# Performance work log

Hardware: AMD Instinct MI355X
Metric: run time of the kernel (lower is better)

## Reference

```python
import jax, jax.numpy as jnp
import numpy as np

B, S = 4, 2048
D_MODEL, N_HEADS, D_KV = 1024, 16, 64
NUM_BUCKETS, MAX_DIST = 32, 128


def _relative_position_bucket(relative_position, num_buckets=NUM_BUCKETS, max_distance=MAX_DIST):
    # bidirectional (encoder) variant, faithful to FlaxT5Attention._relative_position_bucket
    num_buckets = num_buckets // 2
    relative_buckets = (relative_position > 0).astype(jnp.int32) * num_buckets
    rp = jnp.abs(relative_position)
    max_exact = num_buckets // 2
    is_small = rp < max_exact
    rp_large = max_exact + (
        jnp.log(rp.astype(jnp.float32) / max_exact)
        / np.log(max_distance / max_exact)
        * (num_buckets - max_exact)
    )
    rp_large = jnp.minimum(rp_large, num_buckets - 1)
    return relative_buckets + jnp.where(is_small, rp, rp_large.astype(jnp.int32))


def setup_inputs() -> dict:
    key = jax.random.key(0)
    ks = jax.random.split(key, 6)
    return {
        "hidden_states": jax.random.normal(ks[0], (B, S, D_MODEL), jnp.float32),
        "mask": jnp.zeros((B, S), jnp.float32),  # additive mask, 0 = attend
        "wq": jax.random.normal(ks[1], (D_MODEL, N_HEADS * D_KV), jnp.float32) * 0.02,
        "wk": jax.random.normal(ks[2], (D_MODEL, N_HEADS * D_KV), jnp.float32) * 0.02,
        "wv": jax.random.normal(ks[3], (D_MODEL, N_HEADS * D_KV), jnp.float32) * 0.02,
        "wo": jax.random.normal(ks[4], (N_HEADS * D_KV, D_MODEL), jnp.float32) * 0.02,
        "rel_bias": jax.random.normal(ks[5], (NUM_BUCKETS, N_HEADS), jnp.float32) * 0.02,
    }


def reference(hidden_states, mask, wq, wk, wv, wo, rel_bias):
    b, s, _ = hidden_states.shape
    # QKV projections, split heads -> [B, S, H, D]
    q = (hidden_states @ wq).reshape(b, s, N_HEADS, D_KV)
    k = (hidden_states @ wk).reshape(b, s, N_HEADS, D_KV)
    v = (hidden_states @ wv).reshape(b, s, N_HEADS, D_KV)

    # relative position bias -> [1, H, S, S]
    pos = jnp.arange(s, dtype=jnp.int32)
    relative_position = pos[None, :] - pos[:, None]  # memory - query
    buckets = _relative_position_bucket(relative_position)
    position_bias = rel_bias[buckets].transpose(2, 0, 1)[None]  # [1,H,S,S]
    # encoder path: additive mask expanded to [B,1,1,K]
    position_bias = position_bias + mask[:, None, None, :]

    # flax dot_product_attention_weights scales q by 1/sqrt(depth)
    scores = jnp.einsum("bqhd,bkhd->bhqk", q / jnp.sqrt(jnp.float32(D_KV)), k)
    attn_weights = jax.nn.softmax(scores + position_bias, axis=-1)

    attn_output = jnp.einsum("bhqk,bkhd->bqhd", attn_weights, v)
    attn_output = attn_output.reshape(b, s, N_HEADS * D_KV) @ wo
    return attn_output, position_bias
```

## Files before the change

### kernel.cpp

```cpp
#include <hip/hip_runtime.h>
#include <hip/hip_bf16.h>

typedef __attribute__((ext_vector_type(8))) short bf16x8;
typedef __attribute__((ext_vector_type(8))) unsigned short u16x8;
typedef __attribute__((ext_vector_type(4))) float f32x4;

#define B_   4
#define S_   2048
#define H_   16
#define DKV  64
#define DM   1024

static __device__ __forceinline__ f32x4 mfma16(bf16x8 a, bf16x8 b, f32x4 c){
  return __builtin_amdgcn_mfma_f32_16x16x32_bf16(a, b, c, 0, 0, 0);
}
static __device__ __forceinline__ unsigned short f2b(float f){
  union { __hip_bfloat16 b; unsigned short u; } x;
  x.b = __float2bfloat16(f);
  return x.u;
}

__global__ void cast_h_kernel(const float* __restrict__ in, unsigned short* __restrict__ out, int n4){
  int i = blockIdx.x * 256 + threadIdx.x;
  if (i >= n4) return;
  float4 v = reinterpret_cast<const float4*>(in)[i];
  ushort4 r;
  r.x = f2b(v.x); r.y = f2b(v.y); r.z = f2b(v.z); r.w = f2b(v.w);
  reinterpret_cast<ushort4*>(out)[i] = r;
}

__global__ void transpose_w_kernel(const float* __restrict__ w0, const float* __restrict__ w1,
                                   const float* __restrict__ w2, const float* __restrict__ w3,
                                   unsigned short* o0, unsigned short* o1,
                                   unsigned short* o2, unsigned short* o3){
  int z = blockIdx.z;
  const float* src = (z==0) ? w0 : (z==1) ? w1 : (z==2) ? w2 : w3;
  unsigned short* dst = (z==0) ? o0 : (z==1) ? o1 : (z==2) ? o2 : o3;
  __shared__ float tile[32][33];
  int bx = blockIdx.x * 32, by = blockIdx.y * 32;
  int tx = threadIdx.x, ty = threadIdx.y;
  #pragma unroll
  for (int i = 0; i < 32; i += 8)
    tile[ty + i][tx] = src[(size_t)(by + ty + i) * DM + bx + tx];
  __syncthreads();
  #pragma unroll
  for (int i = 0; i < 32; i += 8)
    dst[(size_t)(bx + ty + i) * DM + by + tx] = f2b(tile[tx][ty + i]);
}

__global__ void build_table_kernel(const float* __restrict__ rel_bias, float* __restrict__ table_t){
  int i = blockIdx.x * 256 + threadIdx.x;
  if (i >= 16 * 4095) return;
  int h = i / 4095;
  int idx = i - h * 4095;
  int rel = idx - 2047;
  int bucket = (rel > 0) ? 16 : 0;
  int rp = (rel < 0) ? -rel : rel;
  int off;
  if (rp < 8) off = rp;
  else off = 8 + (rp>=12) + (rp>=16) + (rp>=23) + (rp>=32) + (rp>=46) + (rp>=64) + (rp>=91);
  table_t[i] = rel_bias[(bucket + off) * 16 + h];
}

__global__ void posbias_kernel(const float* __restrict__ relb, const float* __restrict__ mask,
                               float* __restrict__ out){
  __shared__ float rbh[32];
  int row = blockIdx.x;
  int q = row & (S_ - 1);
  int h = (row >> 11) & (H_ - 1);
  int b = row >> 15;
  int tid = threadIdx.x;
  if (tid < 32) rbh[tid] = relb[tid * 16 + h];
  __syncthreads();
  const float* mrow = mask + b * S_;
  float* orow = out + (size_t)row * S_;
  int k0 = tid * 8;
  #pragma unroll
  for (int c = 0; c < 2; ++c){
    float4 mv = *(const float4*)(mrow + k0 + c * 4);
    float4 v;
    #pragma unroll
    for (int j = 0; j < 4; ++j){
      int k = k0 + c * 4 + j;
      int rel = k - q;
      int bucket = (rel > 0) ? 16 : 0;
      int rp = (rel < 0) ? -rel : rel;
      int off = (rp < 8) ? rp
              : 8 + (rp>=12) + (rp>=16) + (rp>=23) + (rp>=32) + (rp>=46) + (rp>=64) + (rp>=91);
      (&v.x)[j] = rbh[bucket + off] + (&mv.x)[j];
    }
    *(float4*)(orow + k0 + c*4) = v;
  }
}

template<int MODE>
__global__ __launch_bounds__(256, 2) void gemm_bt_kernel(
    const unsigned short* __restrict__ A, const unsigned short* __restrict__ Bt,
    void* __restrict__ outp, int M, int N, int K, float scale)
{
  __shared__ __align__(16) unsigned short As[128 * 40];
  __shared__ __align__(16) unsigned short Bs[128 * 40];
  int tid = threadIdx.x; int lane = tid & 63; int w = tid >> 6;
  int wr = w >> 1, wc = w & 1;
  int n0 = blockIdx.x * 128, m0 = blockIdx.y * 128;
  const char* Ab = (const char*)A;
  const char* Bb = (const char*)Bt;
  size_t Kb = (size_t)K * 2;

  int srow = (tid * 16) >> 6;
  int scolb = (tid * 16) & 63;

  f32x4 acc[4][4];
  #pragma unroll
  for (int i = 0; i < 4; ++i)
    #pragma unroll
    for (int j = 0; j < 4; ++j) acc[i][j] = (f32x4){0.f, 0.f, 0.f, 0.f};

  bf16x8 ar[2], br[2];
  auto gload = [&](int kt){
    size_t k0b = (size_t)kt * 64;
    #pragma unroll
    for (int c = 0; c < 2; ++c){
      int row = srow + c * 64;
      ar[c] = *(const bf16x8*)(Ab + (size_t)(m0 + row) * Kb + k0b + scolb);
      br[c] = *(const bf16x8*)(Bb + (size_t)(n0 + row) * Kb + k0b + scolb);
    }
  };
  auto lwrite = [&](){
    #pragma unroll
    for (int c = 0; c < 2; ++c){
      int row = srow + c * 64;
      *(bf16x8*)((char*)As + row * 80 + scolb) = ar[c];
      *(bf16x8*)((char*)Bs + row * 80 + scolb) = br[c];
    }
  };

  int nk = K >> 5;
  gload(0);
  lwrite();
  for (int kt = 0; kt < nk; ++kt){
    __syncthreads();
    if (kt + 1 < nk) gload(kt + 1);
    bf16x8 af[4], bfr[4];
    #pragma unroll
    for (int f = 0; f < 4; ++f){
      int row = wr * 64 + f * 16 + (lane & 15);
      af[f] = *(const bf16x8*)((const char*)As + row * 80 + (lane >> 4) * 16);
    }
    #pragma unroll
    for (int f = 0; f < 4; ++f){
      int row = wc * 64 + f * 16 + (lane & 15);
      bfr[f] = *(const bf16x8*)((const char*)Bs + row * 80 + (lane >> 4) * 16);
    }
    #pragma unroll
    for (int i = 0; i < 4; ++i)
      #pragma unroll
      for (int j = 0; j < 4; ++j)
        acc[i][j] = mfma16(af[i], bfr[j], acc[i][j]);
    __syncthreads();
    if (kt + 1 < nk) lwrite();
  }

  #pragma unroll
  for (int i = 0; i < 4; ++i){
    #pragma unroll
    for (int j = 0; j < 4; ++j){
      #pragma unroll
      for (int r = 0; r < 4; ++r){
        int m = m0 + wr * 64 + i * 16 + ((lane >> 4) * 4) + r;
        int n = n0 + wc * 64 + j * 16 + (lane & 15);
        float v = acc[i][j][r] * scale;
        if (MODE == 0){
          ((float*)outp)[(size_t)m * N + n] = v;
        } else {
          int b = m >> 11, s = m & 2047, hh = n >> 6, d = n & 63;
          ((unsigned short*)outp)[(((size_t)(b * H_ + hh) * S_) + s) * DKV + d] = f2b(v);
        }
      }
    }
  }
}

__global__ __launch_bounds__(256, 2) void attn_mfma_kernel(
    const unsigned short* __restrict__ Qp, const unsigned short* __restrict__ Kp,
    const unsigned short* __restrict__ Vp, const float* __restrict__ table_t,
    const float* __restrict__ mask, unsigned short* __restrict__ outp)
{
  __shared__ __align__(16) unsigned short Ks[64][72];
  __shared__ __align__(16) unsigned short Vs[64][72];
  __shared__ __align__(16) unsigned short Ps[4][16][72];
  __shared__ float bias_s[127];
  __shared__ float mask_s[64];

  int bid = blockIdx.x;
  int qt = bid & 31; int h = (bid >> 5) & 15; int b = bid >> 9;
  int qb = qt * 64;
  const unsigned short* qptr = Qp + ((size_t)(b * H_ + h) * S_ + qb) * DKV;
  const unsigned short* kptr = Kp + (size_t)(b * H_ + h) * S_ * DKV;
  const unsigned short* vptr = Vp + (size_t)(b * H_ + h) * S_ * DKV;
  int tid = threadIdx.x; int lane = tid & 63; int w = tid >> 6;

  bf16x8 qf[2];
  {
    const unsigned short* qrow = qptr + (size_t)(w * 16 + (lane & 15)) * DKV + 8 * (lane >> 4);
    qf[0] = *(const bf16x8*)qrow;
    qf[1] = *(const bf16x8*)(qrow + 32);
  }
  float m_r[4], l_r[4];
  f32x4 o_acc[4];
  #pragma unroll
  for (int r = 0; r < 4; ++r){ m_r[r] = -1e30f; l_r[r] = 0.f; }
  #pragma unroll
  for (int d = 0; d < 4; ++d) o_acc[d] = (f32x4){0.f, 0.f, 0.f, 0.f};

  int bias_base = h * 4095 + (2047 - qb - 63);

  int skey = tid & 63;
  int sd0  = (tid >> 6) * 16;

  for (int k0 = 0; k0 < S_; k0 += 64){
    const unsigned short* krow = kptr + (size_t)(k0 + skey) * DKV + sd0;
    const unsigned short* vrow = vptr + (size_t)(k0 + skey) * DKV + sd0;
    u16x8 ka = *(const u16x8*)krow;
    u16x8 kb2 = *(const u16x8*)(krow + 8);
    u16x8 va = *(const u16x8*)vrow;
    u16x8 vb2 = *(const u16x8*)(vrow + 8);
    float biasr = (tid < 127) ? table_t[bias_base + k0 + tid] : 0.f;
    float maskr = (tid >= 128 && tid < 192) ? mask[b * S_ + k0 + (tid - 128)] : 0.f;

    __syncthreads();
    *(u16x8*)&Ks[skey][sd0]     = ka;
    *(u16x8*)&Ks[skey][sd0 + 8] = kb2;
    #pragma unroll
    for (int j = 0; j < 8; ++j){
      Vs[sd0 + j][skey]     = va[j];
      Vs[sd0 + 8 + j][skey] = vb2[j];
    }
    if (tid < 127) bias_s[tid] = biasr;
    else if (tid < 192) mask_s[tid - 128] = maskr;
    __syncthreads();

    f32x4 sc[4];
    #pragma unroll
    for (int kb = 0; kb < 4; ++kb){
      sc[kb] = (f32x4){0.f, 0.f, 0.f, 0.f};
      #pragma unroll
      for (int ks = 0; ks < 2; ++ks){
        int row = kb * 16 + (lane & 15);
        bf16x8 kf = *(const bf16x8*)&Ks[row][ks * 32 + (lane >> 4) * 8];
        sc[kb] = mfma16(qf[ks], kf, sc[kb]);
      }
    }
    float t[4][4];
    float tmax[4] = {-1e30f, -1e30f, -1e30f, -1e30f};
    #pragma unroll
    for (int kb = 0; kb < 4; ++kb){
      int k_l = kb * 16 + (lane & 15);
      float mk = mask_s[k_l];
      #pragma unroll
      for (int r = 0; r < 4; ++r){
        int q_l = w * 16 + (lane >> 4) * 4 + r;
        float tv = sc[kb][r] + bias_s[k_l - q_l + 63] + mk;
        t[kb][r] = tv;
        tmax[r] = fmaxf(tmax[r], tv);
      }
    }
    #pragma unroll
    for (int r = 0; r < 4; ++r){
      #pragma unroll
      for (int off = 1; off < 16; off <<= 1)
        tmax[r] = fmaxf(tmax[r], __shfl_xor(tmax[r], off, 64));
    }
    float scl[4];
    #pragma unroll
    for (int r = 0; r < 4; ++r){
      float mn = fmaxf(m_r[r], tmax[r]);
      scl[r] = __expf(m_r[r] - mn);
      m_r[r] = mn;
    }
    float rs[4] = {0.f, 0.f, 0.f, 0.f};
    #pragma unroll
    for (int kb = 0; kb < 4; ++kb)
      #pragma unroll
      for (int r = 0; r < 4; ++r){
        float p = __expf(t[kb][r] - m_r[r]);
        t[kb][r] = p;
        rs[r] += p;
      }
    #pragma unroll
    for (int r = 0; r < 4; ++r){
      #pragma unroll
      for (int off = 1; off < 16; off <<= 1)
        rs[r] += __shfl_xor(rs[r], off, 64);
      l_r[r] = l_r[r] * scl[r] + rs[r];
      o_acc[0][r] *= scl[r]; o_acc[1][r] *= scl[r];
      o_acc[2][r] *= scl[r]; o_acc[3][r] *= scl[r];
    }
    #pragma unroll
    for (int kb = 0; kb < 4; ++kb)
      #pragma unroll
      for (int r = 0; r < 4; ++r){
        int prow = (lane >> 4) * 4 + r;
        int pcol = kb * 16 + (lane & 15);
        Ps[w][prow][pcol] = f2b(t[kb][r]);
      }
    bf16x8 pa[2];
    #pragma unroll
    for (int ks = 0; ks < 2; ++ks)
      pa[ks] = *(const bf16x8*)&Ps[w][lane & 15][ks * 32 + (lane >> 4) * 8];
    #pragma unroll
    for (int db = 0; db < 4; ++db)
      #pragma unroll
      for (int ks = 0; ks < 2; ++ks){
        bf16x8 vf = *(const bf16x8*)&Vs[db * 16 + (lane & 15)][ks * 32 + (lane >> 4) * 8];
        o_acc[db] = mfma16(pa[ks], vf, o_acc[db]);
      }
  }

  #pragma unroll
  for (int r = 0; r < 4; ++r){
    float inv = 1.0f / l_r[r];
    int qg = qb + w * 16 + (lane >> 4) * 4 + r;
    size_t rowoff = ((size_t)b * S_ + qg) * DM + h * DKV;
    #pragma unroll
    for (int db = 0; db < 4; ++db)
      outp[rowoff + db * 16 + (lane & 15)] = f2b(o_acc[db][r] * inv);
  }
}

extern "C" void kernel_launch(void* const* d_in, const int* in_sizes, int n_in,
                              void* d_out, int out_size, void* d_ws, size_t ws_size,
                              hipStream_t stream) {
  const float* hs   = (const float*)d_in[0];
  const float* msk  = (const float*)d_in[1];
  const float* wq   = (const float*)d_in[2];
  const float* wk   = (const float*)d_in[3];
  const float* wv   = (const float*)d_in[4];
  const float* wo   = (const float*)d_in[5];
  const float* relb = (const float*)d_in[6];

  float* out_attn = (float*)d_out;
  float* out_pb   = (float*)d_out + (size_t)B_ * S_ * DM;
  char* ws = (char*)out_pb;

  unsigned short* h_bf = (unsigned short*)(ws + 0);
  unsigned short* wq_t = (unsigned short*)(ws + 16777216);
  unsigned short* wk_t = (unsigned short*)(ws + 18874368);
  unsigned short* wv_t = (unsigned short*)(ws + 20971520);
  unsigned short* wo_t = (unsigned short*)(ws + 23068672);
  unsigned short* q_b  = (unsigned short*)(ws + 25165824);
  unsigned short* k_b  = (unsigned short*)(ws + 41943040);
  unsigned short* v_b  = (unsigned short*)(ws + 58720256);
  float*          tabl = (float*)(ws + 75497472);

  cast_h_kernel<<<8192, 256, 0, stream>>>(hs, h_bf, (B_ * S_ * DM) / 4);
  transpose_w_kernel<<<dim3(32, 32, 4), dim3(32, 8), 0, stream>>>(wq, wk, wv, wo,
                                                                  wq_t, wk_t, wv_t, wo_t);
  build_table_kernel<<<256, 256, 0, stream>>>(relb, tabl);

  gemm_bt_kernel<1><<<dim3(8, 64), 256, 0, stream>>>(h_bf, wq_t, q_b, 8192, 1024, 1024, 0.125f);
  gemm_bt_kernel<1><<<dim3(8, 64), 256, 0, stream>>>(h_bf, wk_t, k_b, 8192, 1024, 1024, 1.0f);
  gemm_bt_kernel<1><<<dim3(8, 64), 256, 0, stream>>>(h_bf, wv_t, v_b, 8192, 1024, 1024, 1.0f);

  attn_mfma_kernel<<<B_ * H_ * 32, 256, 0, stream>>>(q_b, k_b, v_b, tabl, msk, h_bf);

  gemm_bt_kernel<0><<<dim3(8, 64), 256, 0, stream>>>(h_bf, wo_t, out_attn, 8192, 1024, 1024, 1.0f);

  posbias_kernel<<<B_ * H_ * S_, 256, 0, stream>>>(relb, msk, out_pb);
}
```

Baseline: 540.8 us.

## Fuse QKV projections into one GEMM and prefetch K/V tiles in attention

```diff
diff --git a/kernel.cpp b/kernel.cpp
--- a/kernel.cpp
+++ b/kernel.cpp
@@ -169,12 +169,14 @@
       for (int r = 0; r < 4; ++r){
         int m = m0 + wr * 64 + i * 16 + ((lane >> 4) * 4) + r;
         int n = n0 + wc * 64 + j * 16 + (lane & 15);
-        float v = acc[i][j][r] * scale;
         if (MODE == 0){
-          ((float*)outp)[(size_t)m * N + n] = v;
+          ((float*)outp)[(size_t)m * N + n] = acc[i][j][r] * scale;
         } else {
-          int b = m >> 11, s = m & 2047, hh = n >> 6, d = n & 63;
-          ((unsigned short*)outp)[(((size_t)(b * H_ + hh) * S_) + s) * DKV + d] = f2b(v);
+          int sel = n >> 10, nn = n & 1023;
+          float v = acc[i][j][r] * (sel == 0 ? 0.125f : 1.0f);
+          int b = m >> 11, s = m & 2047, hh = nn >> 6, d = nn & 63;
+          ((unsigned short*)outp)[(size_t)sel * 8388608 +
+              (((size_t)(b * H_ + hh) * S_) + s) * DKV + d] = f2b(v);
         }
       }
     }
@@ -218,17 +220,19 @@
   int skey = tid & 63;
   int sd0  = (tid >> 6) * 16;
 
-  for (int k0 = 0; k0 < S_; k0 += 64){
+  u16x8 ka, kb2, va, vb2;
+  float biasr = 0.f, maskr = 0.f;
+  auto gload = [&](int k0){
     const unsigned short* krow = kptr + (size_t)(k0 + skey) * DKV + sd0;
     const unsigned short* vrow = vptr + (size_t)(k0 + skey) * DKV + sd0;
-    u16x8 ka = *(const u16x8*)krow;
-    u16x8 kb2 = *(const u16x8*)(krow + 8);
-    u16x8 va = *(const u16x8*)vrow;
-    u16x8 vb2 = *(const u16x8*)(vrow + 8);
-    float biasr = (tid < 127) ? table_t[bias_base + k0 + tid] : 0.f;
-    float maskr = (tid >= 128 && tid < 192) ? mask[b * S_ + k0 + (tid - 128)] : 0.f;
-
-    __syncthreads();
+    ka  = *(const u16x8*)krow;
+    kb2 = *(const u16x8*)(krow + 8);
+    va  = *(const u16x8*)vrow;
+    vb2 = *(const u16x8*)(vrow + 8);
+    if (tid < 127) biasr = table_t[bias_base + k0 + tid];
+    else if (tid >= 128 && tid < 192) maskr = mask[b * S_ + k0 + (tid - 128)];
+  };
+  auto lwrite = [&](){
     *(u16x8*)&Ks[skey][sd0]     = ka;
     *(u16x8*)&Ks[skey][sd0 + 8] = kb2;
     #pragma unroll
@@ -238,7 +242,13 @@
     }
     if (tid < 127) bias_s[tid] = biasr;
     else if (tid < 192) mask_s[tid - 128] = maskr;
+  };
+
+  gload(0);
+  lwrite();
+  for (int k0 = 0; k0 < S_; k0 += 64){
     __syncthreads();
+    if (k0 + 64 < S_) gload(k0 + 64);
 
     f32x4 sc[4];
     #pragma unroll
@@ -315,6 +325,9 @@
         bf16x8 vf = *(const bf16x8*)&Vs[db * 16 + (lane & 15)][ks * 32 + (lane >> 4) * 8];
         o_acc[db] = mfma16(pa[ks], vf, o_acc[db]);
       }
+
+    __syncthreads();
+    if (k0 + 64 < S_) lwrite();
   }
 
   #pragma unroll
@@ -343,26 +356,24 @@
   float* out_pb   = (float*)d_out + (size_t)B_ * S_ * DM;
   char* ws = (char*)out_pb;
 
-  unsigned short* h_bf = (unsigned short*)(ws + 0);
-  unsigned short* wq_t = (unsigned short*)(ws + 16777216);
-  unsigned short* wk_t = (unsigned short*)(ws + 18874368);
-  unsigned short* wv_t = (unsigned short*)(ws + 20971520);
-  unsigned short* wo_t = (unsigned short*)(ws + 23068672);
-  unsigned short* q_b  = (unsigned short*)(ws + 25165824);
-  unsigned short* k_b  = (unsigned short*)(ws + 41943040);
-  unsigned short* v_b  = (unsigned short*)(ws + 58720256);
-  float*          tabl = (float*)(ws + 75497472);
+  unsigned short* h_bf  = (unsigned short*)(ws + 0);
+  unsigned short* wqkv_t= (unsigned short*)(ws + 16777216);
+  unsigned short* wk_t  = (unsigned short*)(ws + 18874368);
+  unsigned short* wv_t  = (unsigned short*)(ws + 20971520);
+  unsigned short* wo_t  = (unsigned short*)(ws + 23068672);
+  unsigned short* qkv_b = (unsigned short*)(ws + 25165824);
+  unsigned short* k_b   = (unsigned short*)(ws + 41943040);
+  unsigned short* v_b   = (unsigned short*)(ws + 58720256);
+  float*          tabl  = (float*)(ws + 75497472);
 
   cast_h_kernel<<<8192, 256, 0, stream>>>(hs, h_bf, (B_ * S_ * DM) / 4);
   transpose_w_kernel<<<dim3(32, 32, 4), dim3(32, 8), 0, stream>>>(wq, wk, wv, wo,
-                                                                  wq_t, wk_t, wv_t, wo_t);
+                                                                  wqkv_t, wk_t, wv_t, wo_t);
   build_table_kernel<<<256, 256, 0, stream>>>(relb, tabl);
 
-  gemm_bt_kernel<1><<<dim3(8, 64), 256, 0, stream>>>(h_bf, wq_t, q_b, 8192, 1024, 1024, 0.125f);
-  gemm_bt_kernel<1><<<dim3(8, 64), 256, 0, stream>>>(h_bf, wk_t, k_b, 8192, 1024, 1024, 1.0f);
-  gemm_bt_kernel<1><<<dim3(8, 64), 256, 0, stream>>>(h_bf, wv_t, v_b, 8192, 1024, 1024, 1.0f);
-
-  attn_mfma_kernel<<<B_ * H_ * 32, 256, 0, stream>>>(q_b, k_b, v_b, tabl, msk, h_bf);
+  gemm_bt_kernel<1><<<dim3(24, 64), 256, 0, stream>>>(h_bf, wqkv_t, qkv_b, 8192, 3072, 1024, 1.0f);
+
+  attn_mfma_kernel<<<B_ * H_ * 32, 256, 0, stream>>>(qkv_b, k_b, v_b, tabl, msk, h_bf);
 
   gemm_bt_kernel<0><<<dim3(8, 64), 256, 0, stream>>>(h_bf, wo_t, out_attn, 8192, 1024, 1024, 1.0f);
 
```

Result: no change. 541.7 us (+0.2%).
